# Performance work log

Hardware: AMD Instinct MI355X
Metric: run time of the kernel (lower is better)

The kernel has to match this reference:

```python
import jax, jax.numpy as jnp
import numpy as np

N = 100000   # nodes
E = 1600000  # edges (avg degree 16)
D_IN = 128
H = 256
D_OUT = 128


def setup_inputs() -> dict:
    key = jax.random.key(0)
    ks = jax.random.split(key, 12)

    def lin_w(k, fan_in, fan_out):
        # torch nn.Linear-style uniform init
        bound = 1.0 / np.sqrt(fan_in)
        return jax.random.uniform(k, (fan_in, fan_out), jnp.float32, -bound, bound)

    return {
        "in_feat": jax.random.normal(ks[0], (N, D_IN), jnp.float32),
        "src": jax.random.randint(ks[1], (E,), 0, N, jnp.int32),
        "dst": jax.random.randint(ks[2], (E,), 0, N, jnp.int32),
        "Wc0": lin_w(ks[3], D_IN, H), "bc0": jnp.zeros((H,), jnp.float32),
        "Wc1": lin_w(ks[4], H, H),    "bc1": jnp.zeros((H,), jnp.float32),
        "Wc2": lin_w(ks[5], H, D_OUT),"bc2": jnp.zeros((D_OUT,), jnp.float32),
        "Wr0": lin_w(ks[6], D_OUT, H),"br0": jnp.zeros((H,), jnp.float32),
        "Wr1": lin_w(ks[7], H, H),    "br1": jnp.zeros((H,), jnp.float32),
        "Wr2": lin_w(ks[8], H, D_IN), "br2": jnp.zeros((D_IN,), jnp.float32),
    }


def _graph_conv(h, src, dst, W, b):
    """DGL GraphConv, norm='both': D_out^{-1/2} A D_in^{-1/2} h W + b."""
    ones = jnp.ones(src.shape[0], h.dtype)
    out_deg = jnp.clip(jax.ops.segment_sum(ones, src, num_segments=N), 1.0)
    in_deg = jnp.clip(jax.ops.segment_sum(ones, dst, num_segments=N), 1.0)
    h = h * (out_deg ** -0.5)[:, None]
    h = h @ W                                    # transform before aggregate
    h = jax.ops.segment_sum(h[src], dst, num_segments=N)  # SpMM aggregation
    return h * (in_deg ** -0.5)[:, None] + b


def reference(in_feat, src, dst, Wc0, bc0, Wc1, bc1, Wc2, bc2,
              Wr0, br0, Wr1, br1, Wr2, br2):
    h = jnp.tanh(_graph_conv(in_feat, src, dst, Wc0, bc0))
    h = jnp.tanh(_graph_conv(h, src, dst, Wc1, bc1))
    h = jax.nn.softmax(_graph_conv(h, src, dst, Wc2, bc2), axis=1)
    r = jnp.tanh(h @ Wr0 + br0)
    r = jnp.tanh(r @ Wr1 + br1)
    r = jax.nn.softmax(r @ Wr2 + br2, axis=1)
    return (h, r)
```

## Files before the change

### kernel.cpp

```cpp
#include <hip/hip_runtime.h>

typedef __attribute__((ext_vector_type(8))) short short8;
typedef __attribute__((ext_vector_type(4))) float f32x4;

__device__ __forceinline__ ushort f2bf(float v) {
    unsigned u = __builtin_bit_cast(unsigned, v);
    unsigned r = (u + 0x7FFFu + ((u >> 16) & 1u)) >> 16;
    return (ushort)r;
}
__device__ __forceinline__ float lo16(unsigned p) { return __builtin_bit_cast(float, p << 16); }
__device__ __forceinline__ float hi16(unsigned p) { return __builtin_bit_cast(float, p & 0xFFFF0000u); }

__device__ __forceinline__ float fast_tanh(float x) {
    float cx = fminf(fmaxf(x, -9.f), 9.f);
    float e = __expf(2.f * cx);
    return (e - 1.f) / (e + 1.f);
}

__device__ __forceinline__ void async16(const void* g, void* l) {
    __builtin_amdgcn_global_load_lds(
        (const __attribute__((address_space(1))) unsigned*)g,
        (__attribute__((address_space(3))) unsigned*)l, 16, 0, 0);
}

#define BSHIFT 9
#define CHUNK 4096

__global__ __launch_bounds__(256) void bucket_count(const int* __restrict__ src,
        const int* __restrict__ dst, int* __restrict__ gbc,
        int* __restrict__ outc, int E) {
    __shared__ int cnt[256];
    int t = threadIdx.x;
    cnt[t] = 0;
    __syncthreads();
    int start = blockIdx.x * CHUNK;
    int n = E - start; if (n > CHUNK) n = CHUNK;
#pragma unroll
    for (int k = 0; k < CHUNK / 256; ++k) {
        int i = t + k * 256;
        if (i < n) {
            atomicAdd(&cnt[dst[start + i] >> BSHIFT], 1);
            atomicAdd(&outc[src[start + i]], 1);
        }
    }
    __syncthreads();
    if (cnt[t]) atomicAdd(&gbc[t], cnt[t]);
}

__global__ void scan_buckets(const int* __restrict__ gbc, int* __restrict__ bucketBase,
                             int* __restrict__ pairCursor, int* __restrict__ roff,
                             int N, int E) {
    __shared__ int s[256];
    int t = threadIdx.x;
    int v = gbc[t];
    s[t] = v; __syncthreads();
    for (int o = 1; o < 256; o <<= 1) {
        int y = (t >= o) ? s[t - o] : 0;
        __syncthreads();
        s[t] += y;
        __syncthreads();
    }
    int excl = s[t] - v;
    bucketBase[t] = excl;
    pairCursor[t] = excl;
    if (t == 255) bucketBase[256] = s[255];
    if (t == 0) roff[N] = E;
}

__global__ __launch_bounds__(256) void part_scatter(const int* __restrict__ src,
        const int* __restrict__ dst, int* __restrict__ pairCursor,
        uint2* __restrict__ pairs, int E) {
    __shared__ int cnt[256];
    __shared__ int base[256];
    int t = threadIdx.x;
    cnt[t] = 0;
    __syncthreads();
    int start = blockIdx.x * CHUNK;
    int n = E - start; if (n > CHUNK) n = CHUNK;
    int sv[CHUNK / 256], dv[CHUNK / 256], rk[CHUNK / 256], bk[CHUNK / 256];
#pragma unroll
    for (int k = 0; k < CHUNK / 256; ++k) {
        int i = t + k * 256;
        if (i < n) {
            sv[k] = src[start + i];
            dv[k] = dst[start + i];
            bk[k] = dv[k] >> BSHIFT;
            rk[k] = atomicAdd(&cnt[bk[k]], 1);
        } else bk[k] = -1;
    }
    __syncthreads();
    base[t] = cnt[t] ? atomicAdd(&pairCursor[t], cnt[t]) : 0;
    __syncthreads();
#pragma unroll
    for (int k = 0; k < CHUNK / 256; ++k)
        if (bk[k] >= 0) pairs[base[bk[k]] + rk[k]] = make_uint2((unsigned)sv[k], (unsigned)dv[k]);
}

__global__ __launch_bounds__(256) void build_bucket(const uint2* __restrict__ pairs,
        const int* __restrict__ bucketBase, int* __restrict__ roff,
        float* __restrict__ sIn, int* __restrict__ csr, int N) {
    __shared__ int cnt[512];
    __shared__ int cur[512];
    __shared__ int ss[256];
    int b = blockIdx.x;
    int t = threadIdx.x;
    int lo = b << BSHIFT;
    int s0 = bucketBase[b], s1 = bucketBase[b + 1];
    cnt[t] = 0; cnt[t + 256] = 0;
    __syncthreads();
    for (int j = s0 + t; j < s1; j += 256)
        atomicAdd(&cnt[pairs[j].y - lo], 1);
    __syncthreads();
    int c0 = cnt[2 * t], c1 = cnt[2 * t + 1];
    ss[t] = c0 + c1; __syncthreads();
    for (int o = 1; o < 256; o <<= 1) {
        int y = (t >= o) ? ss[t - o] : 0;
        __syncthreads();
        ss[t] += y;
        __syncthreads();
    }
    int eb = ss[t] - (c0 + c1);
    int p0 = s0 + eb, p1 = s0 + eb + c0;
    cur[2 * t] = p0; cur[2 * t + 1] = p1;
    int n0 = lo + 2 * t, n1 = n0 + 1;
    if (n0 < N) { roff[n0] = p0; sIn[n0] = rsqrtf((float)(c0 > 0 ? c0 : 1)); }
    if (n1 < N) { roff[n1] = p1; sIn[n1] = rsqrtf((float)(c1 > 0 ? c1 : 1)); }
    __syncthreads();
    for (int j = s0 + t; j < s1; j += 256) {
        uint2 p = pairs[j];
        int pos = atomicAdd(&cur[p.y - lo], 1);
        csr[pos] = (int)p.x;
    }
}

__global__ void convw(const float* w0, const float* w1, const float* w2,
                      const float* w3, const float* w4, const float* w5,
                      ushort* __restrict__ Wt) {
    int i = blockIdx.x * 256 + threadIdx.x;
    int base, Km, Nm; const float* W;
    if      (i < 32768)  { base = 0;      Km = 128; Nm = 256; W = w0; }
    else if (i < 98304)  { base = 32768;  Km = 256; Nm = 256; W = w1; }
    else if (i < 131072) { base = 98304;  Km = 256; Nm = 128; W = w2; }
    else if (i < 163840) { base = 131072; Km = 128; Nm = 256; W = w3; }
    else if (i < 229376) { base = 163840; Km = 256; Nm = 256; W = w4; }
    else                 { base = 229376; Km = 256; Nm = 128; W = w5; }
    int l = i - base;
    int k = l / Nm, n = l % Nm;
    Wt[base + n * Km + k] = f2bf(W[l]);
}

__global__ void prescale(const float* __restrict__ x, const int* __restrict__ outc,
                         ushort* __restrict__ o, float* __restrict__ sOut,
                         int total ) {
    int i = blockIdx.x * 256 + threadIdx.x;
    if (i >= total) return;
    int row = i >> 5;
    int oc = outc[row]; if (oc < 1) oc = 1;
    float s = rsqrtf((float)oc);
    if ((i & 31) == 0) sOut[row] = s;
    float4 v = ((const float4*)x)[i];
    ushort4 r;
    r.x = f2bf(v.x * s); r.y = f2bf(v.y * s);
    r.z = f2bf(v.z * s); r.w = f2bf(v.w * s);
    ((ushort4*)o)[i] = r;
}


__global__ __launch_bounds__(256) void agg128(const ushort* __restrict__ F,
        const int* __restrict__ csr, const int* __restrict__ roff,
        const float* __restrict__ sIn, ushort* __restrict__ out, int N) {
    int w = blockIdx.x * 4 + (threadIdx.x >> 6);
    if (w >= N) return;
    int lane = threadIdx.x & 63;
    int b = roff[w], e = roff[w + 1];
    int deg = e - b;
    int n = deg < 64 ? deg : 64;
    float a0 = 0.f, a1 = 0.f;
    const char* base = (const char*)(F + lane * 2);
    int voff = 0;
    if (n > 0) voff = csr[b + (lane < n ? lane : n - 1)] << 8;
    int j = 0;
    for (; j + 16 <= n; j += 16) {
        unsigned p[16];
#pragma unroll
        for (int k = 0; k < 16; ++k) {
            int o = __shfl(voff, j + k, 64);
            p[k] = *(const unsigned*)(base + (size_t)(unsigned)o);
        }
#pragma unroll
        for (int k = 0; k < 16; ++k) { a0 += lo16(p[k]); a1 += hi16(p[k]); }
    }
    for (; j + 8 <= n; j += 8) {
        unsigned p[8];
#pragma unroll
        for (int k = 0; k < 8; ++k) {
            int o = __shfl(voff, j + k, 64);
            p[k] = *(const unsigned*)(base + (size_t)(unsigned)o);
        }
#pragma unroll
        for (int k = 0; k < 8; ++k) { a0 += lo16(p[k]); a1 += hi16(p[k]); }
    }
    for (; j < n; ++j) {
        int o = __shfl(voff, j, 64);
        unsigned p = *(const unsigned*)(base + (size_t)(unsigned)o);
        a0 += lo16(p); a1 += hi16(p);
    }
    for (int i = b + 64; i < e; ++i) {
        unsigned p = *(const unsigned*)(base + ((size_t)csr[i] << 8));
        a0 += lo16(p); a1 += hi16(p);
    }
    float s = sIn[w];
    ushort2 o2; o2.x = f2bf(a0 * s); o2.y = f2bf(a1 * s);
    *(ushort2*)(out + (size_t)w * 128 + lane * 2) = o2;
}

__global__ __launch_bounds__(256) void agg256(const ushort* __restrict__ F,
        const int* __restrict__ csr, const int* __restrict__ roff,
        const float* __restrict__ sIn, ushort* __restrict__ out, int N) {
    int w = blockIdx.x * 4 + (threadIdx.x >> 6);
    if (w >= N) return;
    int lane = threadIdx.x & 63;
    int b = roff[w], e = roff[w + 1];
    int deg = e - b;
    int n = deg < 64 ? deg : 64;
    float a0 = 0.f, a1 = 0.f, a2 = 0.f, a3 = 0.f;
    const char* base = (const char*)(F + lane * 4);
    int voff = 0;
    if (n > 0) voff = csr[b + (lane < n ? lane : n - 1)] << 9;
    int j = 0;
    for (; j + 16 <= n; j += 16) {
        uint2 p[16];
#pragma unroll
        for (int k = 0; k < 16; ++k) {
            int o = __shfl(voff, j + k, 64);
            p[k] = *(const uint2*)(base + (size_t)(unsigned)o);
        }
#pragma unroll
        for (int k = 0; k < 16; ++k) {
            a0 += lo16(p[k].x); a1 += hi16(p[k].x);
            a2 += lo16(p[k].y); a3 += hi16(p[k].y);
        }
    }
    for (; j + 8 <= n; j += 8) {
        uint2 p[8];
#pragma unroll
        for (int k = 0; k < 8; ++k) {
            int o = __shfl(voff, j + k, 64);
            p[k] = *(const uint2*)(base + (size_t)(unsigned)o);
        }
#pragma unroll
        for (int k = 0; k < 8; ++k) {
            a0 += lo16(p[k].x); a1 += hi16(p[k].x);
            a2 += lo16(p[k].y); a3 += hi16(p[k].y);
        }
    }
    for (; j < n; ++j) {
        int o = __shfl(voff, j, 64);
        uint2 p = *(const uint2*)(base + (size_t)(unsigned)o);
        a0 += lo16(p.x); a1 += hi16(p.x); a2 += lo16(p.y); a3 += hi16(p.y);
    }
    for (int i = b + 64; i < e; ++i) {
        uint2 p = *(const uint2*)(base + ((size_t)csr[i] << 9));
        a0 += lo16(p.x); a1 += hi16(p.x); a2 += lo16(p.y); a3 += hi16(p.y);
    }
    float s = sIn[w];
    ushort4 o4;
    o4.x = f2bf(a0 * s); o4.y = f2bf(a1 * s);
    o4.z = f2bf(a2 * s); o4.w = f2bf(a3 * s);
    *(ushort4*)(out + (size_t)w * 256 + lane * 4) = o4;
}

__global__ __launch_bounds__(256) void agg_softmax(const ushort* __restrict__ F,
        const int* __restrict__ csr, const int* __restrict__ roff,
        const float* __restrict__ sIn, const float* __restrict__ bias,
        float* __restrict__ outh, ushort* __restrict__ outb, int N) {
    int w = blockIdx.x * 4 + (threadIdx.x >> 6);
    if (w >= N) return;
    int lane = threadIdx.x & 63;
    int b = roff[w], e = roff[w + 1];
    int deg = e - b;
    int n = deg < 64 ? deg : 64;
    float a0 = 0.f, a1 = 0.f;
    const char* base = (const char*)(F + lane * 2);
    int voff = 0;
    if (n > 0) voff = csr[b + (lane < n ? lane : n - 1)] << 8;
    int j = 0;
    for (; j + 16 <= n; j += 16) {
        unsigned p[16];
#pragma unroll
        for (int k = 0; k < 16; ++k) {
            int o = __shfl(voff, j + k, 64);
            p[k] = *(const unsigned*)(base + (size_t)(unsigned)o);
        }
#pragma unroll
        for (int k = 0; k < 16; ++k) { a0 += lo16(p[k]); a1 += hi16(p[k]); }
    }
    for (; j + 8 <= n; j += 8) {
        unsigned p[8];
#pragma unroll
        for (int k = 0; k < 8; ++k) {
            int o = __shfl(voff, j + k, 64);
            p[k] = *(const unsigned*)(base + (size_t)(unsigned)o);
        }
#pragma unroll
        for (int k = 0; k < 8; ++k) { a0 += lo16(p[k]); a1 += hi16(p[k]); }
    }
    for (; j < n; ++j) {
        int o = __shfl(voff, j, 64);
        unsigned p = *(const unsigned*)(base + (size_t)(unsigned)o);
        a0 += lo16(p); a1 += hi16(p);
    }
    for (int i = b + 64; i < e; ++i) {
        unsigned p = *(const unsigned*)(base + ((size_t)csr[i] << 8));
        a0 += lo16(p); a1 += hi16(p);
    }
    float s = sIn[w];
    float2 bb = *(const float2*)(bias + lane * 2);
    float l0 = a0 * s + bb.x, l1 = a1 * s + bb.y;
    float m = fmaxf(l0, l1);
    for (int o = 32; o; o >>= 1) m = fmaxf(m, __shfl_xor(m, o, 64));
    float e0 = __expf(l0 - m), e1 = __expf(l1 - m);
    float sm = e0 + e1;
    for (int o = 32; o; o >>= 1) sm += __shfl_xor(sm, o, 64);
    float inv = 1.f / sm;
    float r0 = e0 * inv, r1 = e1 * inv;
    float2 fo; fo.x = r0; fo.y = r1;
    *(float2*)(outh + (size_t)w * 128 + lane * 2) = fo;
    ushort2 o2; o2.x = f2bf(r0); o2.y = f2bf(r1);
    *(ushort2*)(outb + (size_t)w * 128 + lane * 2) = o2;
}

template <int MODE>
__global__ __launch_bounds__(256) void gemm_kernel(
        const ushort* __restrict__ A, const ushort* __restrict__ Wt,
        const float* __restrict__ bias, const float* __restrict__ rowscale,
        void* __restrict__ out, int M, int K, int Nn) {
    __shared__ ushort ldsA[128 * 64];
    __shared__ ushort ldsB[128 * 64];
    const int tid = threadIdx.x;
    const int lane = tid & 63;
    const int wid = tid >> 6;
    const int rowbase = blockIdx.x * 128;
    const int colbase = blockIdx.y * 128;
    const int wr = (wid >> 1) * 64;
    const int wc = (wid & 1) * 64;

    f32x4 acc[4][4];
#pragma unroll
    for (int i = 0; i < 4; ++i)
#pragma unroll
        for (int j = 0; j < 4; ++j) acc[i][j] = (f32x4){0.f, 0.f, 0.f, 0.f};

    const int sr = lane >> 3;
    const int sp = lane & 7;

    for (int kt = 0; kt < K; kt += 64) {
        __syncthreads();
#pragma unroll
        for (int it = 0; it < 4; ++it) {
            int rl = wid * 32 + it * 8 + sr;
            int grow = rowbase + rl; if (grow > M - 1) grow = M - 1;
            int gca = kt + ((sp ^ (rl & 7)) << 3);
            async16(A + (size_t)grow * K + gca, (char*)ldsA + (wid * 32 + it * 8) * 128);
            int gn = colbase + rl;
            int gcb = kt + ((sp ^ (rl & 7)) << 3);
            async16(Wt + (size_t)gn * K + gcb, (char*)ldsB + (wid * 32 + it * 8) * 128);
        }
        __syncthreads();
        const int l15 = lane & 15, l4 = lane >> 4;
#pragma unroll
        for (int ks = 0; ks < 2; ++ks) {
            short8 af[4], bfr[4];
#pragma unroll
            for (int rt = 0; rt < 4; ++rt) {
                int r = wr + rt * 16 + l15;
                int slot = (ks * 4 + l4) ^ (r & 7);
                af[rt] = *(const short8*)&ldsA[r * 64 + slot * 8];
            }
#pragma unroll
            for (int ct = 0; ct < 4; ++ct) {
                int n = wc + ct * 16 + l15;
                int slot = (ks * 4 + l4) ^ (n & 7);
                bfr[ct] = *(const short8*)&ldsB[n * 64 + slot * 8];
            }
#pragma unroll
            for (int rt = 0; rt < 4; ++rt)
#pragma unroll
                for (int ct = 0; ct < 4; ++ct)
                    acc[rt][ct] = __builtin_amdgcn_mfma_f32_16x16x32_bf16(
                        af[rt], bfr[ct], acc[rt][ct], 0, 0, 0);
        }
    }

    const int l15 = lane & 15, l4 = lane >> 4;
    float bv[4];
#pragma unroll
    for (int ct = 0; ct < 4; ++ct)
        bv[ct] = (MODE != 1 && bias) ? bias[colbase + wc + ct * 16 + l15] : 0.f;

    if (MODE != 3) {
#pragma unroll
        for (int rt = 0; rt < 4; ++rt) {
#pragma unroll
            for (int rg = 0; rg < 4; ++rg) {
                int row = rowbase + wr + rt * 16 + l4 * 4 + rg;
                if (row >= M) continue;
                float sc = 1.f;
                if (MODE == 0 && rowscale) sc = rowscale[row];
#pragma unroll
                for (int ct = 0; ct < 4; ++ct) {
                    int col = colbase + wc + ct * 16 + l15;
                    float v = acc[rt][ct][rg] + bv[ct];
                    if (MODE == 0) v = fast_tanh(v) * sc;
                    if (MODE <= 1)
                        ((ushort*)out)[(size_t)row * Nn + col] = f2bf(v);
                    else
                        ((float*)out)[(size_t)row * Nn + col] = v;
                }
            }
        }
    } else {
        __syncthreads();
        float* sred = (float*)ldsA;
#pragma unroll
        for (int rt = 0; rt < 4; ++rt) {
#pragma unroll
            for (int rg = 0; rg < 4; ++rg) {
                float m = acc[rt][0][rg] + bv[0];
#pragma unroll
                for (int ct = 1; ct < 4; ++ct) m = fmaxf(m, acc[rt][ct][rg] + bv[ct]);
                m = fmaxf(m, __shfl_xor(m, 1, 64));
                m = fmaxf(m, __shfl_xor(m, 2, 64));
                m = fmaxf(m, __shfl_xor(m, 4, 64));
                m = fmaxf(m, __shfl_xor(m, 8, 64));
                int row = wr + rt * 16 + l4 * 4 + rg;
                if (l15 == 0) sred[(wid & 1) * 128 + row] = m;
            }
        }
        __syncthreads();
#pragma unroll
        for (int rt = 0; rt < 4; ++rt) {
#pragma unroll
            for (int rg = 0; rg < 4; ++rg) {
                int row = wr + rt * 16 + l4 * 4 + rg;
                float m = fmaxf(sred[row], sred[128 + row]);
                float s = 0.f;
#pragma unroll
                for (int ct = 0; ct < 4; ++ct) {
                    float ev = __expf(acc[rt][ct][rg] + bv[ct] - m);
                    acc[rt][ct][rg] = ev;
                    s += ev;
                }
                s += __shfl_xor(s, 1, 64);
                s += __shfl_xor(s, 2, 64);
                s += __shfl_xor(s, 4, 64);
                s += __shfl_xor(s, 8, 64);
                if (l15 == 0) sred[256 + (wid & 1) * 128 + row] = s;
            }
        }
        __syncthreads();
#pragma unroll
        for (int rt = 0; rt < 4; ++rt) {
#pragma unroll
            for (int rg = 0; rg < 4; ++rg) {
                int row = wr + rt * 16 + l4 * 4 + rg;
                float inv = 1.f / (sred[256 + row] + sred[256 + 128 + row]);
                int grow = rowbase + row;
                if (grow >= M) continue;
#pragma unroll
                for (int ct = 0; ct < 4; ++ct) {
                    int col = colbase + wc + ct * 16 + l15;
                    ((float*)out)[(size_t)grow * Nn + col] = acc[rt][ct][rg] * inv;
                }
            }
        }
    }
}

extern "C" void kernel_launch(void* const* d_in, const int* in_sizes, int n_in,
                              void* d_out, int out_size, void* d_ws, size_t ws_size,
                              hipStream_t stream) {
    (void)n_in; (void)out_size; (void)ws_size;
    const float* in_feat = (const float*)d_in[0];
    const int*   src     = (const int*)d_in[1];
    const int*   dstp    = (const int*)d_in[2];
    const float* Wc0 = (const float*)d_in[3];  const float* bc0 = (const float*)d_in[4];
    const float* Wc1 = (const float*)d_in[5];  const float* bc1 = (const float*)d_in[6];
    const float* Wc2 = (const float*)d_in[7];  const float* bc2 = (const float*)d_in[8];
    const float* Wr0 = (const float*)d_in[9];  const float* br0 = (const float*)d_in[10];
    const float* Wr1 = (const float*)d_in[11]; const float* br1 = (const float*)d_in[12];
    const float* Wr2 = (const float*)d_in[13]; const float* br2 = (const float*)d_in[14];

    const int N = in_sizes[0] / 128;
    const int E = in_sizes[1];
    const int numBuckets = (N + ((1 << BSHIFT) - 1)) >> BSHIFT;

    char* ws = (char*)d_ws;
    size_t off = 0;
    auto alloc = [&](size_t bytes) -> char* {
        char* p = ws + off;
        off += (bytes + 255) & ~(size_t)255;
        return p;
    };
    char* S1 = alloc((size_t)N * 256 * 2);
    char* S2 = alloc((size_t)N * 256 * 2);
    int* csr    = (int*)alloc((size_t)E * 4);
    int* roff   = (int*)alloc((size_t)(N + 1) * 4);
    int* outc   = (int*)alloc((size_t)N * 4);
    float* sOut = (float*)alloc((size_t)N * 4);
    float* sIn  = (float*)alloc((size_t)N * 4);
    ushort* Wt  = (ushort*)alloc(262144 * 2);
    int* gbc        = (int*)alloc(256 * 4);
    int* bucketBase = (int*)alloc(257 * 4);
    int* pairCursor = (int*)alloc(256 * 4);
    uint2* pairs = (uint2*)S2;

    hipMemsetAsync(outc, 0, (size_t)N * 4, stream);
    hipMemsetAsync(gbc, 0, 256 * 4, stream);

    int nblk = (E + CHUNK - 1) / CHUNK;
    bucket_count<<<nblk, 256, 0, stream>>>(src, dstp, gbc, outc, E);
    scan_buckets<<<1, 256, 0, stream>>>(gbc, bucketBase, pairCursor, roff, N, E);
    part_scatter<<<nblk, 256, 0, stream>>>(src, dstp, pairCursor, pairs, E);
    build_bucket<<<numBuckets, 256, 0, stream>>>(pairs, bucketBase, roff, sIn, csr, N);

    convw<<<262144 / 256, 256, 0, stream>>>(Wc0, Wc1, Wc2, Wr0, Wr1, Wr2, Wt);

    ushort* Xs = (ushort*)S1;
    prescale<<<(N * 32 + 255) / 256, 256, 0, stream>>>(in_feat, outc, Xs, sOut, N * 32);

    int aggGrid = (N + 3) / 4;
    dim3 g2((N + 127) / 128, 2), g1((N + 127) / 128, 1);

    ushort* A0 = (ushort*)S2;
    agg128<<<aggGrid, 256, 0, stream>>>(Xs, csr, roff, sIn, A0, N);
    ushort* B1 = (ushort*)S1;
    gemm_kernel<0><<<g2, 256, 0, stream>>>(A0, Wt, bc0, sOut, B1, N, 128, 256);
    ushort* A1 = (ushort*)S2;
    agg256<<<aggGrid, 256, 0, stream>>>(B1, csr, roff, sIn, A1, N);
    ushort* B2 = (ushort*)S1;
    gemm_kernel<0><<<g2, 256, 0, stream>>>(A1, Wt + 32768, bc1, sOut, B2, N, 256, 256);
    ushort* T3 = (ushort*)S2;
    gemm_kernel<1><<<g1, 256, 0, stream>>>(B2, Wt + 98304, nullptr, nullptr, T3, N, 256, 128);
    float* outh = (float*)d_out;
    ushort* Hbf = (ushort*)S1;
    agg_softmax<<<aggGrid, 256, 0, stream>>>(T3, csr, roff, sIn, bc2, outh, Hbf, N);
    ushort* R1 = (ushort*)S2;
    gemm_kernel<0><<<g2, 256, 0, stream>>>(Hbf, Wt + 131072, br0, nullptr, R1, N, 128, 256);
    ushort* R2 = (ushort*)S1;
    gemm_kernel<0><<<g2, 256, 0, stream>>>(R1, Wt + 163840, br1, nullptr, R2, N, 256, 256);
    gemm_kernel<3><<<g1, 256, 0, stream>>>(R2, Wt + 229376, br2, nullptr,
                                           outh + (size_t)N * 128, N, 256, 128);
}
```

Measured before the change: 735.8 us.

## Restructure GEMM to keep full-K weight tile in LDS and A in registers

Replaces the K-looped double-operand LDS GEMM with a kernel templated on K. The full 128xK weight tile is loaded into LDS once, and each wave loads its 32 rows of A straight from global memory into registers. Each wave now covers all 128 output columns, so the softmax epilogue reduces across lanes only and drops its LDS exchange and extra barriers. The aim is fewer barriers and loop iterations and no staging of A through LDS. The cost is more registers, a larger LDS footprint at K=256 (64KB) that may lower occupancy, and uncoalesced direct global loads for A.

```diff
diff --git a/kernel.cpp b/kernel.cpp
--- a/kernel.cpp
+++ b/kernel.cpp
@@ -164,7 +164,6 @@
     r.z = f2bf(v.z * s); r.w = f2bf(v.w * s);
     ((ushort4*)o)[i] = r;
 }
-
 
 __global__ __launch_bounds__(256) void agg128(const ushort* __restrict__ F,
         const int* __restrict__ csr, const int* __restrict__ roff,
@@ -330,147 +329,124 @@
     *(ushort2*)(outb + (size_t)w * 128 + lane * 2) = o2;
 }
 
-template <int MODE>
-__global__ __launch_bounds__(256) void gemm_kernel(
+template <int MODE, int K>
+__global__ __launch_bounds__(256) void gemm2(
         const ushort* __restrict__ A, const ushort* __restrict__ Wt,
         const float* __restrict__ bias, const float* __restrict__ rowscale,
-        void* __restrict__ out, int M, int K, int Nn) {
-    __shared__ ushort ldsA[128 * 64];
-    __shared__ ushort ldsB[128 * 64];
+        void* __restrict__ out, int M, int Nn) {
+    constexpr int SLOTS = K / 8;
+    constexpr int KS = K / 32;
+    constexpr int RPI = 1024 / (2 * K);
+    __shared__ ushort ldsW[128 * K];
+
     const int tid = threadIdx.x;
     const int lane = tid & 63;
     const int wid = tid >> 6;
-    const int rowbase = blockIdx.x * 128;
-    const int colbase = blockIdx.y * 128;
-    const int wr = (wid >> 1) * 64;
-    const int wc = (wid & 1) * 64;
-
-    f32x4 acc[4][4];
-#pragma unroll
-    for (int i = 0; i < 4; ++i)
-#pragma unroll
-        for (int j = 0; j < 4; ++j) acc[i][j] = (f32x4){0.f, 0.f, 0.f, 0.f};
-
-    const int sr = lane >> 3;
-    const int sp = lane & 7;
-
-    for (int kt = 0; kt < K; kt += 64) {
-        __syncthreads();
-#pragma unroll
-        for (int it = 0; it < 4; ++it) {
-            int rl = wid * 32 + it * 8 + sr;
-            int grow = rowbase + rl; if (grow > M - 1) grow = M - 1;
-            int gca = kt + ((sp ^ (rl & 7)) << 3);
-            async16(A + (size_t)grow * K + gca, (char*)ldsA + (wid * 32 + it * 8) * 128);
-            int gn = colbase + rl;
-            int gcb = kt + ((sp ^ (rl & 7)) << 3);
-            async16(Wt + (size_t)gn * K + gcb, (char*)ldsB + (wid * 32 + it * 8) * 128);
-        }
-        __syncthreads();
-        const int l15 = lane & 15, l4 = lane >> 4;
-#pragma unroll
-        for (int ks = 0; ks < 2; ++ks) {
-            short8 af[4], bfr[4];
-#pragma unroll
-            for (int rt = 0; rt < 4; ++rt) {
-                int r = wr + rt * 16 + l15;
-                int slot = (ks * 4 + l4) ^ (r & 7);
-                af[rt] = *(const short8*)&ldsA[r * 64 + slot * 8];
-            }
-#pragma unroll
-            for (int ct = 0; ct < 4; ++ct) {
-                int n = wc + ct * 16 + l15;
-                int slot = (ks * 4 + l4) ^ (n & 7);
-                bfr[ct] = *(const short8*)&ldsB[n * 64 + slot * 8];
-            }
-#pragma unroll
-            for (int rt = 0; rt < 4; ++rt)
-#pragma unroll
-                for (int ct = 0; ct < 4; ++ct)
-                    acc[rt][ct] = __builtin_amdgcn_mfma_f32_16x16x32_bf16(
-                        af[rt], bfr[ct], acc[rt][ct], 0, 0, 0);
-        }
+    const int nby = Nn >> 7;
+    const int bx = (int)blockIdx.x / nby;
+    const int by = (int)blockIdx.x - bx * nby;
+    const int rowbase = bx * 128;
+    const int colbase = by * 128;
+
+#pragma unroll
+    for (int it = 0; it < 128 / (4 * RPI); ++it) {
+        int row0 = it * (4 * RPI) + wid * RPI;
+        int rl = row0 + lane / SLOTS;
+        int sl = lane % SLOTS;
+        int gs = sl ^ (rl & 7);
+        async16(Wt + (size_t)(colbase + rl) * K + gs * 8,
+                (char*)ldsW + row0 * (2 * K));
     }
 
     const int l15 = lane & 15, l4 = lane >> 4;
-    float bv[4];
-#pragma unroll
-    for (int ct = 0; ct < 4; ++ct)
-        bv[ct] = (MODE != 1 && bias) ? bias[colbase + wc + ct * 16 + l15] : 0.f;
+    short8 a[2][KS];
+#pragma unroll
+    for (int rt = 0; rt < 2; ++rt) {
+        int grow = rowbase + wid * 32 + rt * 16 + l15;
+        if (grow > M - 1) grow = M - 1;
+        const ushort* ap = A + (size_t)grow * K + l4 * 8;
+#pragma unroll
+        for (int ks = 0; ks < KS; ++ks)
+            a[rt][ks] = *(const short8*)(ap + ks * 32);
+    }
+
+    f32x4 acc[2][8];
+#pragma unroll
+    for (int i = 0; i < 2; ++i)
+#pragma unroll
+        for (int j = 0; j < 8; ++j) acc[i][j] = (f32x4){0.f, 0.f, 0.f, 0.f};
+
+    __syncthreads();
+
+#pragma unroll
+    for (int ks = 0; ks < KS; ++ks) {
+        short8 b[8];
+#pragma unroll
+        for (int ct = 0; ct < 8; ++ct) {
+            int n = ct * 16 + l15;
+            int slot = (ks * 4 + l4) ^ (n & 7);
+            b[ct] = *(const short8*)&ldsW[n * K + slot * 8];
+        }
+#pragma unroll
+        for (int ct = 0; ct < 8; ++ct) {
+            acc[0][ct] = __builtin_amdgcn_mfma_f32_16x16x32_bf16(a[0][ks], b[ct], acc[0][ct], 0, 0, 0);
+            acc[1][ct] = __builtin_amdgcn_mfma_f32_16x16x32_bf16(a[1][ks], b[ct], acc[1][ct], 0, 0, 0);
+        }
+    }
+
+    float bv[8];
+#pragma unroll
+    for (int ct = 0; ct < 8; ++ct)
+        bv[ct] = (MODE != 1 && bias) ? bias[colbase + ct * 16 + l15] : 0.f;
 
     if (MODE != 3) {
 #pragma unroll
-        for (int rt = 0; rt < 4; ++rt) {
+        for (int rt = 0; rt < 2; ++rt) {
 #pragma unroll
             for (int rg = 0; rg < 4; ++rg) {
-                int row = rowbase + wr + rt * 16 + l4 * 4 + rg;
+                int row = rowbase + wid * 32 + rt * 16 + l4 * 4 + rg;
                 if (row >= M) continue;
                 float sc = 1.f;
                 if (MODE == 0 && rowscale) sc = rowscale[row];
 #pragma unroll
-                for (int ct = 0; ct < 4; ++ct) {
-                    int col = colbase + wc + ct * 16 + l15;
+                for (int ct = 0; ct < 8; ++ct) {
+                    int col = colbase + ct * 16 + l15;
                     float v = acc[rt][ct][rg] + bv[ct];
                     if (MODE == 0) v = fast_tanh(v) * sc;
-                    if (MODE <= 1)
-                        ((ushort*)out)[(size_t)row * Nn + col] = f2bf(v);
-                    else
-                        ((float*)out)[(size_t)row * Nn + col] = v;
+                    ((ushort*)out)[(size_t)row * Nn + col] = f2bf(v);
                 }
             }
         }
     } else {
-        __syncthreads();
-        float* sred = (float*)ldsA;
-#pragma unroll
-        for (int rt = 0; rt < 4; ++rt) {
+#pragma unroll
+        for (int rt = 0; rt < 2; ++rt) {
 #pragma unroll
             for (int rg = 0; rg < 4; ++rg) {
+                int row = rowbase + wid * 32 + rt * 16 + l4 * 4 + rg;
                 float m = acc[rt][0][rg] + bv[0];
 #pragma unroll
-                for (int ct = 1; ct < 4; ++ct) m = fmaxf(m, acc[rt][ct][rg] + bv[ct]);
+                for (int ct = 1; ct < 8; ++ct) m = fmaxf(m, acc[rt][ct][rg] + bv[ct]);
                 m = fmaxf(m, __shfl_xor(m, 1, 64));
                 m = fmaxf(m, __shfl_xor(m, 2, 64));
                 m = fmaxf(m, __shfl_xor(m, 4, 64));
                 m = fmaxf(m, __shfl_xor(m, 8, 64));
-                int row = wr + rt * 16 + l4 * 4 + rg;
-                if (l15 == 0) sred[(wid & 1) * 128 + row] = m;
-            }
-        }
-        __syncthreads();
-#pragma unroll
-        for (int rt = 0; rt < 4; ++rt) {
-#pragma unroll
-            for (int rg = 0; rg < 4; ++rg) {
-                int row = wr + rt * 16 + l4 * 4 + rg;
-                float m = fmaxf(sred[row], sred[128 + row]);
-                float s = 0.f;
-#pragma unroll
-                for (int ct = 0; ct < 4; ++ct) {
-                    float ev = __expf(acc[rt][ct][rg] + bv[ct] - m);
-                    acc[rt][ct][rg] = ev;
-                    s += ev;
+                float ev[8], s = 0.f;
+#pragma unroll
+                for (int ct = 0; ct < 8; ++ct) {
+                    ev[ct] = __expf(acc[rt][ct][rg] + bv[ct] - m);
+                    s += ev[ct];
                 }
                 s += __shfl_xor(s, 1, 64);
                 s += __shfl_xor(s, 2, 64);
                 s += __shfl_xor(s, 4, 64);
                 s += __shfl_xor(s, 8, 64);
-                if (l15 == 0) sred[256 + (wid & 1) * 128 + row] = s;
-            }
-        }
-        __syncthreads();
-#pragma unroll
-        for (int rt = 0; rt < 4; ++rt) {
-#pragma unroll
-            for (int rg = 0; rg < 4; ++rg) {
-                int row = wr + rt * 16 + l4 * 4 + rg;
-                float inv = 1.f / (sred[256 + row] + sred[256 + 128 + row]);
-                int grow = rowbase + row;
-                if (grow >= M) continue;
-#pragma unroll
-                for (int ct = 0; ct < 4; ++ct) {
-                    int col = colbase + wc + ct * 16 + l15;
-                    ((float*)out)[(size_t)grow * Nn + col] = acc[rt][ct][rg] * inv;
+                float inv = 1.f / s;
+                if (row < M) {
+#pragma unroll
+                    for (int ct = 0; ct < 8; ++ct) {
+                        int col = colbase + ct * 16 + l15;
+                        ((float*)out)[(size_t)row * Nn + col] = ev[ct] * inv;
+                    }
                 }
             }
         }
@@ -530,25 +506,25 @@
     prescale<<<(N * 32 + 255) / 256, 256, 0, stream>>>(in_feat, outc, Xs, sOut, N * 32);
 
     int aggGrid = (N + 3) / 4;
-    dim3 g2((N + 127) / 128, 2), g1((N + 127) / 128, 1);
+    int nrb = (N + 127) / 128;
 
     ushort* A0 = (ushort*)S2;
     agg128<<<aggGrid, 256, 0, stream>>>(Xs, csr, roff, sIn, A0, N);
     ushort* B1 = (ushort*)S1;
-    gemm_kernel<0><<<g2, 256, 0, stream>>>(A0, Wt, bc0, sOut, B1, N, 128, 256);
+    gemm2<0, 128><<<nrb * 2, 256, 0, stream>>>(A0, Wt, bc0, sOut, B1, N, 256);
     ushort* A1 = (ushort*)S2;
     agg256<<<aggGrid, 256, 0, stream>>>(B1, csr, roff, sIn, A1, N);
     ushort* B2 = (ushort*)S1;
-    gemm_kernel<0><<<g2, 256, 0, stream>>>(A1, Wt + 32768, bc1, sOut, B2, N, 256, 256);
+    gemm2<0, 256><<<nrb * 2, 256, 0, stream>>>(A1, Wt + 32768, bc1, sOut, B2, N, 256);
     ushort* T3 = (ushort*)S2;
-    gemm_kernel<1><<<g1, 256, 0, stream>>>(B2, Wt + 98304, nullptr, nullptr, T3, N, 256, 128);
+    gemm2<1, 256><<<nrb, 256, 0, stream>>>(B2, Wt + 98304, nullptr, nullptr, T3, N, 128);
     float* outh = (float*)d_out;
     ushort* Hbf = (ushort*)S1;
     agg_softmax<<<aggGrid, 256, 0, stream>>>(T3, csr, roff, sIn, bc2, outh, Hbf, N);
     ushort* R1 = (ushort*)S2;
-    gemm_kernel<0><<<g2, 256, 0, stream>>>(Hbf, Wt + 131072, br0, nullptr, R1, N, 128, 256);
+    gemm2<0, 128><<<nrb * 2, 256, 0, stream>>>(Hbf, Wt + 131072, br0, nullptr, R1, N, 256);
     ushort* R2 = (ushort*)S1;
-    gemm_kernel<0><<<g2, 256, 0, stream>>>(R1, Wt + 163840, br1, nullptr, R2, N, 256, 256);
-    gemm_kernel<3><<<g1, 256, 0, stream>>>(R2, Wt + 229376, br2, nullptr,
-                                           outh + (size_t)N * 128, N, 256, 128);
-}
+    gemm2<0, 256><<<nrb * 2, 256, 0, stream>>>(R1, Wt + 163840, br1, nullptr, R2, N, 256);
+    gemm2<3, 256><<<nrb, 256, 0, stream>>>(R2, Wt + 229376, br2, nullptr,
+                                           outh + (size_t)N * 128, N, 128);
+}
```

Measured after the change: 742.4 us. No clear change (+0.9%).
